# Kernel optimization log

Hardware: AMD Instinct MI355X
Metric: run time of the kernel (lower is better)

The kernel has to match this reference:

```python
import jax, jax.numpy as jnp
import numpy as np

T = 128        # time_sequence_len
H = 64         # time_hidden_size
NOTES = 12
B = 1024       # per-note batch; time-axis batch = NOTES*B
NB = NOTES * B


def setup_inputs() -> dict:
    key = jax.random.key(0)
    ks = jax.random.split(key, 9)
    s = 0.05
    return {
        "x": jax.random.normal(ks[0], (T, NB, 24), jnp.float32),
        # time LSTMCell params (PyTorch layout: W_ih [4H, in], gates order i,f,g,o)
        "W_ih_t": jax.random.normal(ks[1], (4 * H, 24), jnp.float32) * s,
        "W_hh_t": jax.random.normal(ks[2], (4 * H, H), jnp.float32) * s,
        "b_ih_t": jax.random.normal(ks[3], (4 * H,), jnp.float32) * s,
        "b_hh_t": jax.random.normal(ks[4], (4 * H,), jnp.float32) * s,
        # note LSTMCell params: input_size = T*H, hidden = 24
        "W_ih_n": jax.random.normal(ks[5], (4 * 24, T * H), jnp.float32) * s,
        "W_hh_n": jax.random.normal(ks[6], (4 * 24, 24), jnp.float32) * s,
        "b_ih_n": jax.random.normal(ks[7], (4 * 24,), jnp.float32) * s,
        "b_hh_n": jax.random.normal(ks[8], (4 * 24,), jnp.float32) * s,
    }


def _lstm_cell_zero_state(x, W_ih, b_ih, b_hh):
    """nn.LSTMCell applied with h_prev = c_prev = 0 (the source never feeds
    state back, so W_hh @ h_prev == 0 and f-gate * c_prev == 0)."""
    gates = x @ W_ih.T + (b_ih + b_hh)
    i, f, g, o = jnp.split(gates, 4, axis=-1)
    c = jax.nn.sigmoid(i) * jnp.tanh(g)
    return jax.nn.sigmoid(o) * jnp.tanh(c)


def reference(x, W_ih_t, W_hh_t, b_ih_t, b_hh_t, W_ih_n, W_hh_n, b_ih_n, b_hh_n):
    # time axis: every step uses zero state -> batch all T steps at once
    time_outs = _lstm_cell_zero_state(x, W_ih_t, b_ih_t, b_hh_t)  # [T, 12*B, H]
    # rearrange per-note time outputs: [T,12,B,H] -> [12, B, T*H]
    note_in = (time_outs.reshape(T, NOTES, B, H)
               .transpose(1, 2, 0, 3)
               .reshape(NOTES, B, T * H))
    # note axis: again zero-state per step -> batch all 12 notes
    note_outs = _lstm_cell_zero_state(note_in, W_ih_n, b_ih_n, b_hh_n)  # [12, B, 24]
    y_pred = jnp.where(note_outs > 0.5, 1.0, 0.0)
    return y_pred
```

## Files before the change

### kernel.cpp

```cpp
#include <hip/hip_runtime.h>


typedef _Float16 half8  __attribute__((ext_vector_type(8)));
typedef float    f32x4  __attribute__((ext_vector_type(4)));

#define T_STEPS 128
#define NBROWS  12288
#define ROWS_WG 96
#define NRT     128
#define NCOLS   80
#define WN_T_HALF 10240

__device__ inline f32x4 mfma16(half8 a, half8 b, f32x4 c) {
  return __builtin_amdgcn_mfma_f32_16x16x32_f16(a, b, c, 0, 0, 0);
}

__device__ inline void gload_lds16(const _Float16* gsrc, _Float16* ldst) {
  __builtin_amdgcn_global_load_lds(
      (const __attribute__((address_space(1))) void*)gsrc,
      (__attribute__((address_space(3))) void*)ldst, 16, 0, 0);
}

#define SCALE_SIG  -1.4426950408889634f
#define SCALE_TANH  2.8853900817779268f

__global__ __launch_bounds__(256) void k0_prep(
    const float* __restrict__ W_ih_t, const float* __restrict__ b_ih_t,
    const float* __restrict__ b_hh_t, const float* __restrict__ W_ih_n,
    _Float16* __restrict__ wselT_hi, _Float16* __restrict__ wselT_lo,
    _Float16* __restrict__ wnF)
{
  int id = blockIdx.x * 256 + threadIdx.x;
  if (id < 192 * 32) {
    int slot = id >> 5, k = id & 31;
    int ct = slot >> 4, q = slot & 15;
    int kgo = q >> 2, r = q & 3;
    int s = ct * 4 + r;
    int m = s / 3, gidx = s - 3 * m;
    int h = kgo * 16 + m;
    int wrow = (gidx == 0 ? 0 : (gidx == 1 ? 128 : 192)) + h;
    float scale = (gidx == 1) ? SCALE_TANH : SCALE_SIG;
    float v = 0.0f;
    if (k < 24)       v = W_ih_t[wrow * 24 + k] * scale;
    else if (k == 24) v = (b_ih_t[wrow] + b_hh_t[wrow]) * scale;
    _Float16 hi = (_Float16)v;
    wselT_hi[id] = hi;
    wselT_lo[id] = (_Float16)(v - (float)hi);
  }
  for (int e = id; e < T_STEPS * 5120; e += gridDim.x * 256) {
    int t = e / 5120, u = e - t * 5120;
    int nt = u >> 10, u2 = u & 1023;
    int kc = u2 >> 9, u3 = u2 & 511;
    int l = u3 >> 3, j = u3 & 7;
    int cl = l & 15, kg = l >> 4;
    int gcol = nt * 16 + cl;
    int h = kg * 16 + kc * 8 + j;
    float v = 0.0f;
    if (gcol < 72) {
      int wr = (gcol < 24) ? gcol : gcol + 24;
      v = W_ih_n[(size_t)wr * 8192 + t * 64 + h];
    }
    _Float16 hi = (_Float16)v;
    size_t base = (size_t)t * WN_T_HALF + nt * 2048 + kc * 1024 + u3;
    wnF[base]       = hi;
    wnF[base + 512] = (_Float16)(v - (float)hi);
  }
}

__global__ __launch_bounds__(192, 2)
void k1_time_note(
    const float* __restrict__ x,
    const _Float16* __restrict__ wselT,
    const _Float16* __restrict__ wnF,
    float* __restrict__ partials, int tchunk)
{
  __shared__ _Float16 wsl[12288];

  const int tid = threadIdx.x;
  const int l   = tid & 63;
  const int w   = tid >> 6;
  const int cl  = l & 15;
  const int kg  = l >> 4;

  const int rt   = blockIdx.x % NRT;
  const int ts   = blockIdx.x / NRT;
  const int row0 = rt * ROWS_WG;
  const int t0   = ts * tchunk;

#pragma unroll
  for (int i = 0; i < 8; ++i) {
    int c = i * 3 + w;
    gload_lds16(wselT + c * 512 + l * 8, wsl + c * 512);
  }

  f32x4 nacc[2][5];
#pragma unroll
  for (int mt = 0; mt < 2; ++mt)
#pragma unroll
    for (int nt = 0; nt < 5; ++nt)
      nacc[mt][nt] = (f32x4){0.f, 0.f, 0.f, 0.f};

  const size_t xrow[2] = {
    (size_t)(row0 + w * 32 + 0  + cl) * 24 + kg * 8,
    (size_t)(row0 + w * 32 + 16 + cl) * 24 + kg * 8 };
  const bool xok = (kg < 3);

  float xcur[2][8];
#pragma unroll
  for (int mt = 0; mt < 2; ++mt) {
    f32x4 a = {0,0,0,0}, b = {0,0,0,0};
    if (xok) {
      const float* g = x + (size_t)t0 * NBROWS * 24 + xrow[mt];
      a = *(const f32x4*)g;
      b = *(const f32x4*)(g + 4);
    }
#pragma unroll
    for (int q = 0; q < 4; ++q) { xcur[mt][q] = a[q]; xcur[mt][4 + q] = b[q]; }
    if (!xok) xcur[mt][0] = 1.0f;
  }
  __syncthreads();

  for (int tt = 0; tt < tchunk; ++tt) {
    const int t = t0 + tt;
    int tg = t + 1; if (tg > T_STEPS - 1) tg = T_STEPS - 1;
    const _Float16* wnbase = wnF + (size_t)t * WN_T_HALF + l * 8;

    half8 xh[2], xl[2];
#pragma unroll
    for (int mt = 0; mt < 2; ++mt)
#pragma unroll
      for (int q = 0; q < 8; ++q) {
        _Float16 h = (_Float16)xcur[mt][q];
        xh[mt][q] = h;
        xl[mt][q] = (_Float16)(xcur[mt][q] - (float)h);
      }

    half8 tah[2][2], tal[2][2];
    float xnxt[2][8];

#pragma unroll
    for (int kk = 0; kk < 4; ++kk) {
      f32x4 g[2][3];
#pragma unroll
      for (int c = 0; c < 3; ++c) {
        int woff = ((kk * 3 + c) * 16 + cl) * 32 + kg * 8;
        half8 wh = *(half8*)&wsl[woff];
        half8 wl2 = *(half8*)&wsl[6144 + woff];
#pragma unroll
        for (int mt = 0; mt < 2; ++mt) {
          f32x4 a = (f32x4){0.f, 0.f, 0.f, 0.f};
          a = mfma16(wh,  xh[mt], a);
          a = mfma16(wh,  xl[mt], a);
          a = mfma16(wl2, xh[mt], a);
          g[mt][c] = a;
        }
      }
#pragma unroll
      for (int mt = 0; mt < 2; ++mt)
#pragma unroll
        for (int mq = 0; mq < 4; ++mq) {
          const int ls = 3 * mq;
          float zi = g[mt][(ls)     >> 2][(ls)     & 3];
          float zg = g[mt][(ls + 1) >> 2][(ls + 1) & 3];
          float zo = g[mt][(ls + 2) >> 2][(ls + 2) & 3];
          float Ei = __builtin_amdgcn_exp2f(zi);
          float Eg = __builtin_amdgcn_exp2f(zg);
          float Eo = __builtin_amdgcn_exp2f(zo);
          float d1 = (1.0f + Ei) * (1.0f + Eg);
          float cp = (SCALE_TANH * Eg - SCALE_TANH) * __builtin_amdgcn_rcpf(d1);
          float Ec = __builtin_amdgcn_exp2f(cp);
          float d2 = (1.0f + Eo) * (1.0f + Ec);
          float to = (Ec - 1.0f) * __builtin_amdgcn_rcpf(d2);
          _Float16 th = (_Float16)to;
          _Float16 tl = (_Float16)(to - (float)th);
          const int m = kk * 4 + mq;
          tah[mt][m >> 3][m & 7] = th;
          tal[mt][m >> 3][m & 7] = tl;
        }

      if (kk == 1) {
        half8 bh[5], bl[5];
#pragma unroll
        for (int nt = 0; nt < 5; ++nt) {
          bh[nt] = *(const half8*)(wnbase + nt * 2048);
          bl[nt] = *(const half8*)(wnbase + nt * 2048 + 512);
        }
        __builtin_amdgcn_s_setprio(1);
#pragma unroll
        for (int nt = 0; nt < 5; ++nt)
#pragma unroll
          for (int mt = 0; mt < 2; ++mt) {
            nacc[mt][nt] = mfma16(tah[mt][0], bh[nt], nacc[mt][nt]);
            nacc[mt][nt] = mfma16(tah[mt][0], bl[nt], nacc[mt][nt]);
            nacc[mt][nt] = mfma16(tal[mt][0], bh[nt], nacc[mt][nt]);
          }
        __builtin_amdgcn_s_setprio(0);
#pragma unroll
        for (int mt = 0; mt < 2; ++mt) {
          f32x4 a = {0,0,0,0}, b = {0,0,0,0};
          if (xok) {
            const float* gp = x + (size_t)tg * NBROWS * 24 + xrow[mt];
            a = *(const f32x4*)gp;
            b = *(const f32x4*)(gp + 4);
          }
#pragma unroll
          for (int q = 0; q < 4; ++q) { xnxt[mt][q] = a[q]; xnxt[mt][4+q] = b[q]; }
          if (!xok) xnxt[mt][0] = 1.0f;
        }
      }
    }

    {
      half8 bh[5], bl[5];
#pragma unroll
      for (int nt = 0; nt < 5; ++nt) {
        bh[nt] = *(const half8*)(wnbase + nt * 2048 + 1024);
        bl[nt] = *(const half8*)(wnbase + nt * 2048 + 1024 + 512);
      }
      __builtin_amdgcn_s_setprio(1);
#pragma unroll
      for (int nt = 0; nt < 5; ++nt)
#pragma unroll
        for (int mt = 0; mt < 2; ++mt) {
          nacc[mt][nt] = mfma16(tah[mt][1], bh[nt], nacc[mt][nt]);
          nacc[mt][nt] = mfma16(tah[mt][1], bl[nt], nacc[mt][nt]);
          nacc[mt][nt] = mfma16(tal[mt][1], bh[nt], nacc[mt][nt]);
        }
      __builtin_amdgcn_s_setprio(0);
    }

#pragma unroll
    for (int mt = 0; mt < 2; ++mt)
#pragma unroll
      for (int q = 0; q < 8; ++q) xcur[mt][q] = xnxt[mt][q];
  }

  float* pbase = partials + (size_t)ts * NBROWS * NCOLS;
#pragma unroll
  for (int mt = 0; mt < 2; ++mt)
#pragma unroll
    for (int nt = 0; nt < 5; ++nt)
#pragma unroll
      for (int r = 0; r < 4; ++r) {
        int row = row0 + w * 32 + mt * 16 + kg * 4 + r;
        int col = nt * 16 + cl;
        pbase[(size_t)row * NCOLS + col] = nacc[mt][nt][r];
      }
}

__global__ __launch_bounds__(256) void k2_note_out(
    const float* __restrict__ partials,
    const float* __restrict__ b_ih_n, const float* __restrict__ b_hh_n,
    float* __restrict__ out, int tsplit)
{
  int idx = blockIdx.x * 256 + threadIdx.x;
  if (idx >= NBROWS * 24) return;
  int row = idx / 24, jj = idx - row * 24;
  float gi = 0.f, gg = 0.f, go = 0.f;
  for (int p = 0; p < tsplit; ++p) {
    const float* pp = partials + ((size_t)p * NBROWS + row) * NCOLS;
    gi += pp[jj];
    gg += pp[24 + jj];
    go += pp[48 + jj];
  }
  gi += b_ih_n[jj]      + b_hh_n[jj];
  gg += b_ih_n[48 + jj] + b_hh_n[48 + jj];
  go += b_ih_n[72 + jj] + b_hh_n[72 + jj];
  float si = 1.f / (1.f + expf(-gi));
  float so = 1.f / (1.f + expf(-go));
  float v = so * tanhf(si * tanhf(gg));
  out[idx] = (v > 0.5f) ? 1.0f : 0.0f;
}

extern "C" void kernel_launch(void* const* d_in, const int* in_sizes, int n_in,
                              void* d_out, int out_size, void* d_ws, size_t ws_size,
                              hipStream_t stream)
{
  (void)in_sizes; (void)n_in; (void)out_size;
  const float* x      = (const float*)d_in[0];
  const float* W_ih_t = (const float*)d_in[1];
  const float* b_ih_t = (const float*)d_in[3];
  const float* b_hh_t = (const float*)d_in[4];
  const float* W_ih_n = (const float*)d_in[5];
  const float* b_ih_n = (const float*)d_in[7];
  const float* b_hh_n = (const float*)d_in[8];
  float* out = (float*)d_out;

  char* ws = (char*)d_ws;
  _Float16* wselT_hi = (_Float16*)(ws + 0);
  _Float16* wselT_lo = (_Float16*)(ws + 12288);
  _Float16* wnF      = (_Float16*)(ws + 32768);
  float*    partials = (float*)   (ws + 4194304);

  int tsplit = 8;
  while (tsplit > 1 &&
         4194304ull + (size_t)tsplit * NBROWS * NCOLS * 4 > ws_size)
    tsplit >>= 1;
  int tchunk = T_STEPS / tsplit;

  k0_prep<<<dim3(512), dim3(256), 0, stream>>>(
      W_ih_t, b_ih_t, b_hh_t, W_ih_n, wselT_hi, wselT_lo, wnF);

  k1_time_note<<<dim3(NRT * tsplit), dim3(192), 0, stream>>>(
      x, wselT_hi, wnF, partials, tchunk);

  k2_note_out<<<dim3((NBROWS * 24 + 255) / 256), dim3(256), 0, stream>>>(
      partials, b_ih_n, b_hh_n, out, tsplit);
}
```

Measured before the change: 164.8 us.

## Use 4-wave workgroups, double the time split, and prefetch note weights earlier

The kernel now uses 256 threads (4 waves, 128 rows) per workgroup with 96 row tiles, and the time split goes from 8 to 16 chunks. The per-step body moves into a helper unrolled by two with ping-pong x buffers. The first half of the note weights is loaded at step start and the second half is issued right after the first note MFMA batch, so global loads overlap compute. Doubling the time split also doubles the partials that k2 has to reduce and adds workspace pressure.

```diff
diff --git a/kernel.cpp b/kernel.cpp
--- a/kernel.cpp
+++ b/kernel.cpp
@@ -6,8 +6,8 @@
 
 #define T_STEPS 128
 #define NBROWS  12288
-#define ROWS_WG 96
-#define NRT     128
+#define ROWS_WG 128
+#define NRT     96
 #define NCOLS   80
 #define WN_T_HALF 10240
 
@@ -67,7 +67,118 @@
   }
 }
 
-__global__ __launch_bounds__(192, 2)
+__device__ __forceinline__ void t_step(
+    int t, int tg, float (*xc)[8], float (*xn)[8],
+    const float* __restrict__ x, const _Float16* __restrict__ wnF,
+    const _Float16* wsl, const size_t* xrow, bool xok,
+    int cl, int kg, int l, f32x4 (*nacc)[5])
+{
+  const _Float16* wn_t = wnF + (size_t)t * WN_T_HALF + l * 8;
+
+  half8 b0h[5], b0l[5];
+#pragma unroll
+  for (int nt = 0; nt < 5; ++nt) {
+    b0h[nt] = *(const half8*)(wn_t + nt * 2048);
+    b0l[nt] = *(const half8*)(wn_t + nt * 2048 + 512);
+  }
+
+  half8 xh[2], xl[2];
+#pragma unroll
+  for (int mt = 0; mt < 2; ++mt)
+#pragma unroll
+    for (int q = 0; q < 8; ++q) {
+      _Float16 h = (_Float16)xc[mt][q];
+      xh[mt][q] = h;
+      xl[mt][q] = (_Float16)(xc[mt][q] - (float)h);
+    }
+
+  half8 ta0h[2], ta0l[2], ta1h[2], ta1l[2];
+  half8 b1h[5], b1l[5];
+
+#pragma unroll
+  for (int kk = 0; kk < 4; ++kk) {
+    f32x4 g[2][3];
+#pragma unroll
+    for (int c = 0; c < 3; ++c) {
+      int woff = ((kk * 3 + c) * 16 + cl) * 32 + kg * 8;
+      half8 wh  = *(const half8*)&wsl[woff];
+      half8 wl2 = *(const half8*)&wsl[6144 + woff];
+#pragma unroll
+      for (int mt = 0; mt < 2; ++mt) {
+        f32x4 a = (f32x4){0.f, 0.f, 0.f, 0.f};
+        a = mfma16(wh,  xh[mt], a);
+        a = mfma16(wh,  xl[mt], a);
+        a = mfma16(wl2, xh[mt], a);
+        g[mt][c] = a;
+      }
+    }
+#pragma unroll
+    for (int mt = 0; mt < 2; ++mt)
+#pragma unroll
+      for (int mq = 0; mq < 4; ++mq) {
+        const int ls = 3 * mq;
+        float zi = g[mt][(ls)     >> 2][(ls)     & 3];
+        float zg = g[mt][(ls + 1) >> 2][(ls + 1) & 3];
+        float zo = g[mt][(ls + 2) >> 2][(ls + 2) & 3];
+        float Ei = __builtin_amdgcn_exp2f(zi);
+        float Eg = __builtin_amdgcn_exp2f(zg);
+        float Eo = __builtin_amdgcn_exp2f(zo);
+        float d1 = (1.0f + Ei) * (1.0f + Eg);
+        float cp = (SCALE_TANH * Eg - SCALE_TANH) * __builtin_amdgcn_rcpf(d1);
+        float Ec = __builtin_amdgcn_exp2f(cp);
+        float d2 = (1.0f + Eo) * (1.0f + Ec);
+        float to = (Ec - 1.0f) * __builtin_amdgcn_rcpf(d2);
+        _Float16 th = (_Float16)to;
+        _Float16 tl = (_Float16)(to - (float)th);
+        const int m = kk * 4 + mq;
+        if (kk < 2) { ta0h[mt][m]     = th; ta0l[mt][m]     = tl; }
+        else        { ta1h[mt][m - 8] = th; ta1l[mt][m - 8] = tl; }
+      }
+
+    if (kk == 1) {
+      __builtin_amdgcn_s_setprio(1);
+#pragma unroll
+      for (int nt = 0; nt < 5; ++nt)
+#pragma unroll
+        for (int mt = 0; mt < 2; ++mt) {
+          nacc[mt][nt] = mfma16(ta0h[mt], b0h[nt], nacc[mt][nt]);
+          nacc[mt][nt] = mfma16(ta0h[mt], b0l[nt], nacc[mt][nt]);
+          nacc[mt][nt] = mfma16(ta0l[mt], b0h[nt], nacc[mt][nt]);
+        }
+      __builtin_amdgcn_s_setprio(0);
+#pragma unroll
+      for (int nt = 0; nt < 5; ++nt) {
+        b1h[nt] = *(const half8*)(wn_t + nt * 2048 + 1024);
+        b1l[nt] = *(const half8*)(wn_t + nt * 2048 + 1536);
+      }
+#pragma unroll
+      for (int mt = 0; mt < 2; ++mt) {
+        f32x4 a = {0, 0, 0, 0}, b = {0, 0, 0, 0};
+        if (xok) {
+          const float* gp = x + (size_t)tg * NBROWS * 24 + xrow[mt];
+          a = *(const f32x4*)gp;
+          b = *(const f32x4*)(gp + 4);
+        }
+#pragma unroll
+        for (int q = 0; q < 4; ++q) { xn[mt][q] = a[q]; xn[mt][4 + q] = b[q]; }
+        if (!xok) xn[mt][0] = 1.0f;
+      }
+    }
+  }
+
+  __builtin_amdgcn_s_setprio(1);
+#pragma unroll
+  for (int nt = 0; nt < 5; ++nt)
+#pragma unroll
+    for (int mt = 0; mt < 2; ++mt) {
+      nacc[mt][nt] = mfma16(ta1h[mt], b1h[nt], nacc[mt][nt]);
+      nacc[mt][nt] = mfma16(ta1h[mt], b1l[nt], nacc[mt][nt]);
+      nacc[mt][nt] = mfma16(ta1l[mt], b1h[nt], nacc[mt][nt]);
+    }
+  __builtin_amdgcn_s_setprio(0);
+}
+
+__global__ __launch_bounds__(256, 2)
 void k1_time_note(
     const float* __restrict__ x,
     const _Float16* __restrict__ wselT,
@@ -88,8 +199,8 @@
   const int t0   = ts * tchunk;
 
 #pragma unroll
-  for (int i = 0; i < 8; ++i) {
-    int c = i * 3 + w;
+  for (int i = 0; i < 6; ++i) {
+    int c = i * 4 + w;
     gload_lds16(wselT + c * 512 + l * 8, wsl + c * 512);
   }
 
@@ -105,134 +216,26 @@
     (size_t)(row0 + w * 32 + 16 + cl) * 24 + kg * 8 };
   const bool xok = (kg < 3);
 
-  float xcur[2][8];
+  float xA[2][8], xB[2][8];
 #pragma unroll
   for (int mt = 0; mt < 2; ++mt) {
-    f32x4 a = {0,0,0,0}, b = {0,0,0,0};
+    f32x4 a = {0, 0, 0, 0}, b = {0, 0, 0, 0};
     if (xok) {
       const float* g = x + (size_t)t0 * NBROWS * 24 + xrow[mt];
       a = *(const f32x4*)g;
       b = *(const f32x4*)(g + 4);
     }
 #pragma unroll
-    for (int q = 0; q < 4; ++q) { xcur[mt][q] = a[q]; xcur[mt][4 + q] = b[q]; }
-    if (!xok) xcur[mt][0] = 1.0f;
+    for (int q = 0; q < 4; ++q) { xA[mt][q] = a[q]; xA[mt][4 + q] = b[q]; }
+    if (!xok) xA[mt][0] = 1.0f;
   }
   __syncthreads();
 
-  for (int tt = 0; tt < tchunk; ++tt) {
-    const int t = t0 + tt;
-    int tg = t + 1; if (tg > T_STEPS - 1) tg = T_STEPS - 1;
-    const _Float16* wnbase = wnF + (size_t)t * WN_T_HALF + l * 8;
-
-    half8 xh[2], xl[2];
-#pragma unroll
-    for (int mt = 0; mt < 2; ++mt)
-#pragma unroll
-      for (int q = 0; q < 8; ++q) {
-        _Float16 h = (_Float16)xcur[mt][q];
-        xh[mt][q] = h;
-        xl[mt][q] = (_Float16)(xcur[mt][q] - (float)h);
-      }
-
-    half8 tah[2][2], tal[2][2];
-    float xnxt[2][8];
-
-#pragma unroll
-    for (int kk = 0; kk < 4; ++kk) {
-      f32x4 g[2][3];
-#pragma unroll
-      for (int c = 0; c < 3; ++c) {
-        int woff = ((kk * 3 + c) * 16 + cl) * 32 + kg * 8;
-        half8 wh = *(half8*)&wsl[woff];
-        half8 wl2 = *(half8*)&wsl[6144 + woff];
-#pragma unroll
-        for (int mt = 0; mt < 2; ++mt) {
-          f32x4 a = (f32x4){0.f, 0.f, 0.f, 0.f};
-          a = mfma16(wh,  xh[mt], a);
-          a = mfma16(wh,  xl[mt], a);
-          a = mfma16(wl2, xh[mt], a);
-          g[mt][c] = a;
-        }
-      }
-#pragma unroll
-      for (int mt = 0; mt < 2; ++mt)
-#pragma unroll
-        for (int mq = 0; mq < 4; ++mq) {
-          const int ls = 3 * mq;
-          float zi = g[mt][(ls)     >> 2][(ls)     & 3];
-          float zg = g[mt][(ls + 1) >> 2][(ls + 1) & 3];
-          float zo = g[mt][(ls + 2) >> 2][(ls + 2) & 3];
-          float Ei = __builtin_amdgcn_exp2f(zi);
-          float Eg = __builtin_amdgcn_exp2f(zg);
-          float Eo = __builtin_amdgcn_exp2f(zo);
-          float d1 = (1.0f + Ei) * (1.0f + Eg);
-          float cp = (SCALE_TANH * Eg - SCALE_TANH) * __builtin_amdgcn_rcpf(d1);
-          float Ec = __builtin_amdgcn_exp2f(cp);
-          float d2 = (1.0f + Eo) * (1.0f + Ec);
-          float to = (Ec - 1.0f) * __builtin_amdgcn_rcpf(d2);
-          _Float16 th = (_Float16)to;
-          _Float16 tl = (_Float16)(to - (float)th);
-          const int m = kk * 4 + mq;
-          tah[mt][m >> 3][m & 7] = th;
-          tal[mt][m >> 3][m & 7] = tl;
-        }
-
-      if (kk == 1) {
-        half8 bh[5], bl[5];
-#pragma unroll
-        for (int nt = 0; nt < 5; ++nt) {
-          bh[nt] = *(const half8*)(wnbase + nt * 2048);
-          bl[nt] = *(const half8*)(wnbase + nt * 2048 + 512);
-        }
-        __builtin_amdgcn_s_setprio(1);
-#pragma unroll
-        for (int nt = 0; nt < 5; ++nt)
-#pragma unroll
-          for (int mt = 0; mt < 2; ++mt) {
-            nacc[mt][nt] = mfma16(tah[mt][0], bh[nt], nacc[mt][nt]);
-            nacc[mt][nt] = mfma16(tah[mt][0], bl[nt], nacc[mt][nt]);
-            nacc[mt][nt] = mfma16(tal[mt][0], bh[nt], nacc[mt][nt]);
-          }
-        __builtin_amdgcn_s_setprio(0);
-#pragma unroll
-        for (int mt = 0; mt < 2; ++mt) {
-          f32x4 a = {0,0,0,0}, b = {0,0,0,0};
-          if (xok) {
-            const float* gp = x + (size_t)tg * NBROWS * 24 + xrow[mt];
-            a = *(const f32x4*)gp;
-            b = *(const f32x4*)(gp + 4);
-          }
-#pragma unroll
-          for (int q = 0; q < 4; ++q) { xnxt[mt][q] = a[q]; xnxt[mt][4+q] = b[q]; }
-          if (!xok) xnxt[mt][0] = 1.0f;
-        }
-      }
-    }
-
-    {
-      half8 bh[5], bl[5];
-#pragma unroll
-      for (int nt = 0; nt < 5; ++nt) {
-        bh[nt] = *(const half8*)(wnbase + nt * 2048 + 1024);
-        bl[nt] = *(const half8*)(wnbase + nt * 2048 + 1024 + 512);
-      }
-      __builtin_amdgcn_s_setprio(1);
-#pragma unroll
-      for (int nt = 0; nt < 5; ++nt)
-#pragma unroll
-        for (int mt = 0; mt < 2; ++mt) {
-          nacc[mt][nt] = mfma16(tah[mt][1], bh[nt], nacc[mt][nt]);
-          nacc[mt][nt] = mfma16(tah[mt][1], bl[nt], nacc[mt][nt]);
-          nacc[mt][nt] = mfma16(tal[mt][1], bh[nt], nacc[mt][nt]);
-        }
-      __builtin_amdgcn_s_setprio(0);
-    }
-
-#pragma unroll
-    for (int mt = 0; mt < 2; ++mt)
-#pragma unroll
-      for (int q = 0; q < 8; ++q) xcur[mt][q] = xnxt[mt][q];
+  for (int tt = 0; tt < tchunk; tt += 2) {
+    int ta = t0 + tt, tb = ta + 1;
+    int tg2 = (tt + 2 < tchunk) ? (tb + 1) : tb;
+    t_step(ta, tb,  xA, xB, x, wnF, wsl, xrow, xok, cl, kg, l, nacc);
+    t_step(tb, tg2, xB, xA, x, wnF, wsl, xrow, xok, cl, kg, l, nacc);
   }
 
   float* pbase = partials + (size_t)ts * NBROWS * NCOLS;
@@ -292,7 +295,7 @@
   _Float16* wnF      = (_Float16*)(ws + 32768);
   float*    partials = (float*)   (ws + 4194304);
 
-  int tsplit = 8;
+  int tsplit = 16;
   while (tsplit > 1 &&
          4194304ull + (size_t)tsplit * NBROWS * NCOLS * 4 > ws_size)
     tsplit >>= 1;
@@ -301,7 +304,7 @@
   k0_prep<<<dim3(512), dim3(256), 0, stream>>>(
       W_ih_t, b_ih_t, b_hh_t, W_ih_n, wselT_hi, wselT_lo, wnF);
 
-  k1_time_note<<<dim3(NRT * tsplit), dim3(192), 0, stream>>>(
+  k1_time_note<<<dim3(NRT * tsplit), dim3(256), 0, stream>>>(
       x, wselT_hi, wnF, partials, tchunk);
 
   k2_note_out<<<dim3((NBROWS * 24 + 255) / 256), dim3(256), 0, stream>>>(
```

After: 141.1 us. -14.4%, faster.
